# Kernel optimization log

Hardware: AMD Instinct MI355X
Metric: run time of the kernel (lower is better)

Reference implementation:

```python
import jax, jax.numpy as jnp
import numpy as np
from jax import lax

HIDDEN = 256
HORIZON = 168  # 7 * 24


def _cell(x, h, c, Wih, Whh, bih, bhh):
    # PyTorch LSTM cell: gate order i, f, g, o
    gates = x @ Wih.T + bih + h @ Whh.T + bhh  # [B, 4*HIDDEN]
    i, f, g, o = jnp.split(gates, 4, axis=-1)
    c = jax.nn.sigmoid(f) * c + jax.nn.sigmoid(i) * jnp.tanh(g)
    h = jax.nn.sigmoid(o) * jnp.tanh(c)
    return h, c


def setup_inputs() -> dict:
    key = jax.random.key(0)
    ks = jax.random.split(key, 20)
    B, T, H = 1024, 336, HIDDEN
    s = 0.05

    def p(k, shape):
        return jax.random.normal(k, shape, dtype=jnp.float32) * s

    inp = {"x": jax.random.normal(ks[0], (B, T), dtype=jnp.float32)}
    # encoder layer 0 (input_size=1), layer 1 (input=HIDDEN)
    inp["enc_Wih0"] = p(ks[1], (4 * H, 1)); inp["enc_Whh0"] = p(ks[2], (4 * H, H))
    inp["enc_bih0"] = p(ks[3], (4 * H,)); inp["enc_bhh0"] = p(ks[4], (4 * H,))
    inp["enc_Wih1"] = p(ks[5], (4 * H, H)); inp["enc_Whh1"] = p(ks[6], (4 * H, H))
    inp["enc_bih1"] = p(ks[7], (4 * H,)); inp["enc_bhh1"] = p(ks[8], (4 * H,))
    # decoder layers
    inp["dec_Wih0"] = p(ks[9], (4 * H, 1)); inp["dec_Whh0"] = p(ks[10], (4 * H, H))
    inp["dec_bih0"] = p(ks[11], (4 * H,)); inp["dec_bhh0"] = p(ks[12], (4 * H,))
    inp["dec_Wih1"] = p(ks[13], (4 * H, H)); inp["dec_Whh1"] = p(ks[14], (4 * H, H))
    inp["dec_bih1"] = p(ks[15], (4 * H,)); inp["dec_bhh1"] = p(ks[16], (4 * H,))
    # final projection hidden -> 1
    inp["fc_W"] = p(ks[17], (1, H)); inp["fc_b"] = p(ks[18], (1,))
    return inp


def reference(x, enc_Wih0, enc_Whh0, enc_bih0, enc_bhh0,
              enc_Wih1, enc_Whh1, enc_bih1, enc_bhh1,
              dec_Wih0, dec_Whh0, dec_bih0, dec_bhh0,
              dec_Wih1, dec_Whh1, dec_bih1, dec_bhh1,
              fc_W, fc_b):
    B = x.shape[0]
    xs = x[:, :, None].transpose(1, 0, 2)  # [T, B, 1]
    z = jnp.zeros((B, HIDDEN), dtype=x.dtype)

    def enc_step(carry, xt):
        h0, c0, h1, c1 = carry
        h0, c0 = _cell(xt, h0, c0, enc_Wih0, enc_Whh0, enc_bih0, enc_bhh0)
        h1, c1 = _cell(h0, h1, c1, enc_Wih1, enc_Whh1, enc_bih1, enc_bhh1)
        return (h0, c0, h1, c1), None

    (h0, c0, h1, c1), _ = lax.scan(enc_step, (z, z, z, z), xs)

    dec_inp = x[:, -1:]  # [B, 1] last observed value

    def dec_step(carry, _):
        h0, c0, h1, c1, inp = carry
        h0, c0 = _cell(inp, h0, c0, dec_Wih0, dec_Whh0, dec_bih0, dec_bhh0)
        h1, c1 = _cell(h0, h1, c1, dec_Wih1, dec_Whh1, dec_bih1, dec_bhh1)
        pred = h1 @ fc_W.T + fc_b  # [B, 1]
        return (h0, c0, h1, c1, pred), pred

    _, preds = lax.scan(dec_step, (h0, c0, h1, c1, dec_inp), None, length=HORIZON)
    return preds[:, :, 0].T  # [B, HORIZON]
```

## Files before the change

kernel.cpp:

```cpp
#include <hip/hip_runtime.h>

#define HIDDEN 256
#define TENC 336
#define HORIZ 168
#define BSZ 1024
#define BH (BSZ*HIDDEN)

typedef _Float16 f16;
typedef f16 f16x8 __attribute__((ext_vector_type(8)));
typedef float f32x4 __attribute__((ext_vector_type(4)));
typedef unsigned int u32;
typedef unsigned long long u64;

#define H0_OFF 0
#define H1_OFF (2*BH*2)
#define PP_OFF (H1_OFF + 2*BH*2)
#define CNT_OFF (PP_OFF + BSZ*16*4)
#define WS_TOTAL (CNT_OFF + 16*128)

#define LDS_A0 0
#define LDS_A1 32768
#define LDS_X0 65536
#define XSTRIDE 18
#define LDS_X1 (LDS_X0 + 256*XSTRIDE*4)
#define LDS_SM (LDS_X1 + 256*XSTRIDE*4)
#define LDS_TOTAL (LDS_SM + 1024)

__device__ __forceinline__ float sigm(float x){ return 1.0f/(1.0f+__expf(-x)); }
__device__ __forceinline__ float tanh_f(float x){ return 2.0f/(1.0f+__expf(-2.0f*x)) - 1.0f; }

__device__ __forceinline__ u64 ald64(const void* p){
  return __hip_atomic_load((const u64*)p, __ATOMIC_RELAXED, __HIP_MEMORY_SCOPE_AGENT);
}
__device__ __forceinline__ u32 ald32(const u32* p){
  return __hip_atomic_load(p, __ATOMIC_RELAXED, __HIP_MEMORY_SCOPE_AGENT);
}
__device__ __forceinline__ void ast32(u32* p, u32 v){
  __hip_atomic_store(p, v, __ATOMIC_RELAXED, __HIP_MEMORY_SCOPE_AGENT);
}

__device__ __forceinline__ f16x8 loadWfrag(const float* W, int grow, int k){
  const float* p = W + grow*HIDDEN + k;
  float4 lo = *(const float4*)p;
  float4 hi = *(const float4*)(p+4);
  f16x8 r;
  r[0]=(f16)lo.x; r[1]=(f16)lo.y; r[2]=(f16)lo.z; r[3]=(f16)lo.w;
  r[4]=(f16)hi.x; r[5]=(f16)hi.y; r[6]=(f16)hi.z; r[7]=(f16)hi.w;
  return r;
}

__device__ __forceinline__ const f16* slot_src(const f16* base, int g, int s){
  int l = s & 63, f = s >> 6;
  int kt = f >> 2, mt = f & 3;
  int row = g*64 + mt*16 + (l&15);
  int k = kt*32 + 8*(l>>4);
  return base + row*HIDDEN + k;
}

__device__ __forceinline__ void stage_tile(char* dst, const f16* src_base, int g, int tid){
  u64 v[8];
  #pragma unroll
  for (int i=0;i<4;++i){
    const f16* src = slot_src(src_base, g, tid + 512*i);
    v[2*i]   = ald64(src);
    v[2*i+1] = ald64(src+4);
  }
  #pragma unroll
  for (int i=0;i<4;++i){
    int s = tid + 512*i;
    *(u64*)(dst + s*16)     = v[2*i];
    *(u64*)(dst + s*16 + 8) = v[2*i+1];
  }
}

__device__ __forceinline__ void stage2(char* dA, const f16* sA, char* dB, const f16* sB,
                                       int g, int tid){
  u64 va[8], vb[8];
  #pragma unroll
  for (int i=0;i<4;++i){
    const f16* src = slot_src(sA, g, tid + 512*i);
    va[2*i]   = ald64(src);
    va[2*i+1] = ald64(src+4);
  }
  #pragma unroll
  for (int i=0;i<4;++i){
    const f16* src = slot_src(sB, g, tid + 512*i);
    vb[2*i]   = ald64(src);
    vb[2*i+1] = ald64(src+4);
  }
  #pragma unroll
  for (int i=0;i<4;++i){
    int s = tid + 512*i;
    *(u64*)(dA + s*16)     = va[2*i];
    *(u64*)(dA + s*16 + 8) = va[2*i+1];
    *(u64*)(dB + s*16)     = vb[2*i];
    *(u64*)(dB + s*16 + 8) = vb[2*i+1];
  }
}

__device__ __forceinline__ void cellpair(const float* X, const float* bs, const float* wih, float xr,
                                         int crow, int dp, float& ca, float& cb, float& hA, float& hB){
  float iA = X[(0*64+crow)*XSTRIDE+dp  ] + bs[dp]      + xr*wih[dp];
  float iB = X[(0*64+crow)*XSTRIDE+dp+1] + bs[dp+1]    + xr*wih[dp+1];
  float fA = X[(1*64+crow)*XSTRIDE+dp  ] + bs[16+dp]   + xr*wih[16+dp];
  float fB = X[(1*64+crow)*XSTRIDE+dp+1] + bs[16+dp+1] + xr*wih[16+dp+1];
  float gA = X[(2*64+crow)*XSTRIDE+dp  ] + bs[32+dp]   + xr*wih[32+dp];
  float gB = X[(2*64+crow)*XSTRIDE+dp+1] + bs[32+dp+1] + xr*wih[32+dp+1];
  float oA = X[(3*64+crow)*XSTRIDE+dp  ] + bs[48+dp]   + xr*wih[48+dp];
  float oB = X[(3*64+crow)*XSTRIDE+dp+1] + bs[48+dp+1] + xr*wih[48+dp+1];
  ca = sigm(fA)*ca + sigm(iA)*tanh_f(gA);
  cb = sigm(fB)*cb + sigm(iB)*tanh_f(gB);
  hA = sigm(oA)*tanh_f(ca);
  hB = sigm(oB)*tanh_f(cb);
}

__device__ __forceinline__ void storeh(f16* base, int rowg, int col, float hA, float hB){
  u32 pk = (u32)__builtin_bit_cast(unsigned short, (f16)hA)
         | ((u32)__builtin_bit_cast(unsigned short, (f16)hB) << 16);
  ast32((u32*)(base + rowg*HIDDEN + col), pk);
}

__device__ __forceinline__ void gbar(u32* cnt, int tid, u32 target){
  __syncthreads();
  if (tid == 0)
    (void)__hip_atomic_fetch_add(cnt, 1u, __ATOMIC_RELAXED, __HIP_MEMORY_SCOPE_AGENT);
  if (tid < 64){
    for (int it = 0; it < (1<<17); ++it){
      if (ald32(cnt) >= target) break;
    }
  }
  __syncthreads();
}

struct P {
  const float *x;
  const float *eWih0,*eWhh0,*eBih0,*eBhh0,*eWih1,*eWhh1,*eBih1,*eBhh1;
  const float *dWih0,*dWhh0,*dBih0,*dBhh0,*dWih1,*dWhh1,*dBih1,*dBhh1;
  const float *fcW,*fcB;
  float* out;
  char* ws;
};

__global__ void initk(char* ws){
  u32* p = (u32*)ws;
  size_t total = (size_t)WS_TOTAL / 4;
  for (size_t k = (size_t)blockIdx.x*blockDim.x + threadIdx.x; k < total;
       k += (size_t)gridDim.x*blockDim.x) p[k] = 0u;
}

__global__ __launch_bounds__(512, 2) void lstm_main(P p){
  const int tid  = threadIdx.x;
  const int lane = tid & 63;
  const int w    = tid >> 6;
  const int n    = w & 3;
  const int mh   = w >> 2;
  const int blk  = blockIdx.x;
  const int g    = blk & 15;
  const int j    = blk >> 4;

  extern __shared__ __align__(16) char smem[];
  char*  A0 = smem + LDS_A0;
  char*  A1 = smem + LDS_A1;
  float* X0 = (float*)(smem + LDS_X0);
  float* X1 = (float*)(smem + LDS_X1);
  float* wih0s = (float*)(smem + LDS_SM);
  float* b0s   = wih0s + 64;
  float* b1s   = wih0s + 128;
  float* fcWs  = wih0s + 192;
  float* fcbs  = wih0s + 208;

  f16*   h0buf = (f16*)(p.ws + H0_OFF);
  f16*   h1buf = (f16*)(p.ws + H1_OFF);
  float* ppart = (float*)(p.ws + PP_OFF);
  u32*   cnt   = (u32*)(p.ws + CNT_OFF) + g*32;

  const int crow = tid >> 3;
  const int dp   = (tid & 7) * 2;
  const int rowg = g*64 + crow;
  const int cold = j*16 + dp;

  float c0a=0.f, c0b=0.f, c1a=0.f, c1b=0.f;

  if (tid < 64){
    int gt = tid >> 4, d = tid & 15;
    int grow = gt*256 + j*16 + d;
    wih0s[tid] = p.eWih0[grow];
    b0s[tid] = p.eBih0[grow] + p.eBhh0[grow];
    b1s[tid] = p.eBih1[grow] + p.eBhh1[grow];
  }
  if (tid < 16) fcWs[tid] = p.fcW[j*16 + tid];
  if (tid == 0) fcbs[0] = p.fcB[0];

  f16x8 B0[8], B1i[8], B1h[8];
  {
    int grow = n*256 + j*16 + (lane & 15);
    int kb = 8*(lane>>4);
    #pragma unroll
    for (int kt=0; kt<8; ++kt){
      B0[kt]  = loadWfrag(p.eWhh0, grow, kt*32 + kb);
      B1i[kt] = loadWfrag(p.eWih1, grow, kt*32 + kb);
      B1h[kt] = loadWfrag(p.eWhh1, grow, kt*32 + kb);
    }
  }
  __syncthreads();

  u32 ev = 0;

  for (int r = 0; r <= TENC; ++r){
    float xr = (r < TENC) ? p.x[rowg*TENC + r] : 0.f;
    stage2(A0, h0buf + ((r+1)&1)*BH, A1, h1buf + (r&1)*BH, g, tid);
    __syncthreads();

    f32x4 acc0[2] = {{0.f,0.f,0.f,0.f},{0.f,0.f,0.f,0.f}};
    f32x4 acc1[2] = {{0.f,0.f,0.f,0.f},{0.f,0.f,0.f,0.f}};
    #pragma unroll
    for (int kt=0; kt<8; ++kt){
      #pragma unroll
      for (int m=0; m<2; ++m){
        f16x8 a = *(const f16x8*)(A0 + ((kt*4 + (mh*2+m))*64 + lane)*16);
        acc0[m] = __builtin_amdgcn_mfma_f32_16x16x32_f16(a, B0[kt],  acc0[m], 0,0,0);
        acc1[m] = __builtin_amdgcn_mfma_f32_16x16x32_f16(a, B1i[kt], acc1[m], 0,0,0);
      }
    }
    #pragma unroll
    for (int kt=0; kt<8; ++kt){
      #pragma unroll
      for (int m=0; m<2; ++m){
        f16x8 a = *(const f16x8*)(A1 + ((kt*4 + (mh*2+m))*64 + lane)*16);
        acc1[m] = __builtin_amdgcn_mfma_f32_16x16x32_f16(a, B1h[kt], acc1[m], 0,0,0);
      }
    }

    #pragma unroll
    for (int m=0; m<2; ++m){
      int rb = mh*32 + m*16 + 4*(lane>>4);
      #pragma unroll
      for (int q=0; q<4; ++q){
        X0[(n*64 + rb + q)*XSTRIDE + (lane&15)] = acc0[m][q];
        X1[(n*64 + rb + q)*XSTRIDE + (lane&15)] = acc1[m][q];
      }
    }
    __syncthreads();

    if (r < TENC){
      float hA, hB;
      cellpair(X0, b0s, wih0s, xr, crow, dp, c0a, c0b, hA, hB);
      storeh(h0buf + (r&1)*BH, rowg, cold, hA, hB);
    }
    if (r >= 1){
      float hA, hB;
      cellpair(X1, b1s, wih0s, 0.f, crow, dp, c1a, c1b, hA, hB);
      storeh(h1buf + ((r-1)&1)*BH, rowg, cold, hA, hB);
    }
    ++ev;
    gbar(cnt, tid, 16u*ev);
  }

  __syncthreads();
  if (tid < 64){
    int gt = tid >> 4, d = tid & 15;
    int grow = gt*256 + j*16 + d;
    wih0s[tid] = p.dWih0[grow];
    b0s[tid] = p.dBih0[grow] + p.dBhh0[grow];
    b1s[tid] = p.dBih1[grow] + p.dBhh1[grow];
  }
  {
    int grow = n*256 + j*16 + (lane & 15);
    int kb = 8*(lane>>4);
    #pragma unroll
    for (int kt=0; kt<8; ++kt){
      B0[kt]  = loadWfrag(p.dWhh0, grow, kt*32 + kb);
      B1i[kt] = loadWfrag(p.dWih1, grow, kt*32 + kb);
      B1h[kt] = loadWfrag(p.dWhh1, grow, kt*32 + kb);
    }
  }
  __syncthreads();

  for (int t = 0; t < HORIZ; ++t){
    u64 ppv = 0;
    float xlast = 0.f;
    if (t == 0) xlast = p.x[rowg*TENC + (TENC-1)];
    else        ppv   = ald64(ppart + rowg*16 + (tid&7)*2);

    stage2(A0, h0buf + ((t+1)&1)*BH, A1, h1buf + ((t+1)&1)*BH, g, tid);
    __syncthreads();

    f32x4 acc0[2] = {{0.f,0.f,0.f,0.f},{0.f,0.f,0.f,0.f}};
    f32x4 acc1[2] = {{0.f,0.f,0.f,0.f},{0.f,0.f,0.f,0.f}};
    #pragma unroll
    for (int kt=0; kt<8; ++kt){
      #pragma unroll
      for (int m=0; m<2; ++m){
        f16x8 a0 = *(const f16x8*)(A0 + ((kt*4 + (mh*2+m))*64 + lane)*16);
        acc0[m] = __builtin_amdgcn_mfma_f32_16x16x32_f16(a0, B0[kt],  acc0[m], 0,0,0);
        f16x8 a1 = *(const f16x8*)(A1 + ((kt*4 + (mh*2+m))*64 + lane)*16);
        acc1[m] = __builtin_amdgcn_mfma_f32_16x16x32_f16(a1, B1h[kt], acc1[m], 0,0,0);
      }
    }
    #pragma unroll
    for (int m=0; m<2; ++m){
      int rb = mh*32 + m*16 + 4*(lane>>4);
      #pragma unroll
      for (int q=0; q<4; ++q) X0[(n*64 + rb + q)*XSTRIDE + (lane&15)] = acc0[m][q];
    }
    __syncthreads();

    float inp;
    if (t == 0){
      inp = xlast;
    } else {
      float a = __builtin_bit_cast(float, (u32)(ppv & 0xffffffffull));
      float b = __builtin_bit_cast(float, (u32)(ppv >> 32));
      float s = a + b;
      s += __shfl_xor(s, 1);
      s += __shfl_xor(s, 2);
      s += __shfl_xor(s, 4);
      inp = s + fcbs[0];
    }
    {
      float hA, hB;
      cellpair(X0, b0s, wih0s, inp, crow, dp, c0a, c0b, hA, hB);
      storeh(h0buf + (t&1)*BH, rowg, cold, hA, hB);
    }
    if (t > 0 && j == 0 && (tid & 7) == 0) p.out[rowg*HORIZ + (t-1)] = inp;
    ++ev;
    gbar(cnt, tid, 16u*ev);

    stage_tile(A0, h0buf + (t&1)*BH, g, tid);
    __syncthreads();

    #pragma unroll
    for (int kt=0; kt<8; ++kt){
      #pragma unroll
      for (int m=0; m<2; ++m){
        f16x8 a0 = *(const f16x8*)(A0 + ((kt*4 + (mh*2+m))*64 + lane)*16);
        acc1[m] = __builtin_amdgcn_mfma_f32_16x16x32_f16(a0, B1i[kt], acc1[m], 0,0,0);
      }
    }
    #pragma unroll
    for (int m=0; m<2; ++m){
      int rb = mh*32 + m*16 + 4*(lane>>4);
      #pragma unroll
      for (int q=0; q<4; ++q) X1[(n*64 + rb + q)*XSTRIDE + (lane&15)] = acc1[m][q];
    }
    __syncthreads();

    {
      float hA, hB;
      cellpair(X1, b1s, wih0s, 0.f, crow, dp, c1a, c1b, hA, hB);
      storeh(h1buf + (t&1)*BH, rowg, cold, hA, hB);
      float pp = fcWs[dp]*hA + fcWs[dp+1]*hB;
      pp += __shfl_xor(pp, 1);
      pp += __shfl_xor(pp, 2);
      pp += __shfl_xor(pp, 4);
      if ((tid & 7) == 0)
        ast32((u32*)(ppart + rowg*16 + j), __builtin_bit_cast(u32, pp));
    }
    ++ev;
    gbar(cnt, tid, 16u*ev);
  }

  if (j == 0){
    u64 ppv = ald64(ppart + rowg*16 + (tid&7)*2);
    float a = __builtin_bit_cast(float, (u32)(ppv & 0xffffffffull));
    float b = __builtin_bit_cast(float, (u32)(ppv >> 32));
    float s = a + b;
    s += __shfl_xor(s, 1);
    s += __shfl_xor(s, 2);
    s += __shfl_xor(s, 4);
    if ((tid & 7) == 0) p.out[rowg*HORIZ + (HORIZ-1)] = s + fcbs[0];
  }
}

extern "C" void kernel_launch(void* const* d_in, const int* in_sizes, int n_in,
                              void* d_out, int out_size, void* d_ws, size_t ws_size,
                              hipStream_t stream) {
  (void)in_sizes; (void)n_in; (void)out_size;
  if (ws_size < (size_t)WS_TOTAL) return;

  P prm;
  prm.x     = (const float*)d_in[0];
  prm.eWih0 = (const float*)d_in[1];  prm.eWhh0 = (const float*)d_in[2];
  prm.eBih0 = (const float*)d_in[3];  prm.eBhh0 = (const float*)d_in[4];
  prm.eWih1 = (const float*)d_in[5];  prm.eWhh1 = (const float*)d_in[6];
  prm.eBih1 = (const float*)d_in[7];  prm.eBhh1 = (const float*)d_in[8];
  prm.dWih0 = (const float*)d_in[9];  prm.dWhh0 = (const float*)d_in[10];
  prm.dBih0 = (const float*)d_in[11]; prm.dBhh0 = (const float*)d_in[12];
  prm.dWih1 = (const float*)d_in[13]; prm.dWhh1 = (const float*)d_in[14];
  prm.dBih1 = (const float*)d_in[15]; prm.dBhh1 = (const float*)d_in[16];
  prm.fcW   = (const float*)d_in[17]; prm.fcB   = (const float*)d_in[18];
  prm.out   = (float*)d_out;
  prm.ws    = (char*)d_ws;

  hipLaunchKernelGGL(initk, dim3(512), dim3(256), 0, stream, (char*)d_ws);

  hipFuncSetAttribute((const void*)lstm_main,
                      hipFuncAttributeMaxDynamicSharedMemorySize, LDS_TOTAL);
  void* args[] = { &prm };
  hipLaunchCooperativeKernel((const void*)lstm_main, dim3(256), dim3(512),
                             args, LDS_TOTAL, stream);
}
```

Baseline: 4.034 ms.

## Replace atomic-counter barrier with per-block flags and pre-convert weights to fp16

```diff
diff --git a/kernel.cpp b/kernel.cpp
--- a/kernel.cpp
+++ b/kernel.cpp
@@ -5,6 +5,7 @@
 #define HORIZ 168
 #define BSZ 1024
 #define BH (BSZ*HIDDEN)
+#define WMAT (1024*256)
 
 typedef _Float16 f16;
 typedef f16 f16x8 __attribute__((ext_vector_type(8)));
@@ -15,13 +16,15 @@
 #define H0_OFF 0
 #define H1_OFF (2*BH*2)
 #define PP_OFF (H1_OFF + 2*BH*2)
-#define CNT_OFF (PP_OFF + BSZ*16*4)
-#define WS_TOTAL (CNT_OFF + 16*128)
+#define FLAG_OFF (PP_OFF + BSZ*16*4)
+#define WS_BASE (FLAG_OFF + 16*16*64)
+#define WF16_OFF WS_BASE
+#define WS_FULL (WF16_OFF + 6*WMAT*2)
 
 #define LDS_A0 0
 #define LDS_A1 32768
 #define LDS_X0 65536
-#define XSTRIDE 18
+#define XSTRIDE 16
 #define LDS_X1 (LDS_X0 + 256*XSTRIDE*4)
 #define LDS_SM (LDS_X1 + 256*XSTRIDE*4)
 #define LDS_TOTAL (LDS_SM + 1024)
@@ -120,13 +123,13 @@
   ast32((u32*)(base + rowg*HIDDEN + col), pk);
 }
 
-__device__ __forceinline__ void gbar(u32* cnt, int tid, u32 target){
+__device__ __forceinline__ void gbar(u32* gf, int j, int lane, int tid, u32 ev){
   __syncthreads();
-  if (tid == 0)
-    (void)__hip_atomic_fetch_add(cnt, 1u, __ATOMIC_RELAXED, __HIP_MEMORY_SCOPE_AGENT);
-  if (tid < 64){
+  if (tid == 0) ast32(gf + j*16, ev);
+  if (tid < 64 && lane < 16){
+    const u32* sp = gf + lane*16;
     for (int it = 0; it < (1<<17); ++it){
-      if (ald32(cnt) >= target) break;
+      if (__all((int)(ald32(sp) >= ev))) break;
     }
   }
   __syncthreads();
@@ -139,16 +142,32 @@
   const float *fcW,*fcB;
   float* out;
   char* ws;
+  int usef16;
+};
+
+struct WC {
+  const float* src0; const float* src1; const float* src2;
+  const float* src3; const float* src4; const float* src5;
+  f16* dst;
 };
 
 __global__ void initk(char* ws){
   u32* p = (u32*)ws;
-  size_t total = (size_t)WS_TOTAL / 4;
+  size_t total = (size_t)WS_BASE / 4;
   for (size_t k = (size_t)blockIdx.x*blockDim.x + threadIdx.x; k < total;
        k += (size_t)gridDim.x*blockDim.x) p[k] = 0u;
 }
 
-__global__ __launch_bounds__(512, 2) void lstm_main(P p){
+__global__ void wconv(WC wc){
+  int m = blockIdx.y;
+  const float* s = (m==0)?wc.src0:(m==1)?wc.src1:(m==2)?wc.src2:
+                   (m==3)?wc.src3:(m==4)?wc.src4:wc.src5;
+  f16* d = wc.dst + (size_t)m*WMAT;
+  for (int i = blockIdx.x*blockDim.x + threadIdx.x; i < WMAT;
+       i += gridDim.x*blockDim.x) d[i] = (f16)s[i];
+}
+
+__global__ __launch_bounds__(512) void lstm_main(P p){
   const int tid  = threadIdx.x;
   const int lane = tid & 63;
   const int w    = tid >> 6;
@@ -172,7 +191,8 @@
   f16*   h0buf = (f16*)(p.ws + H0_OFF);
   f16*   h1buf = (f16*)(p.ws + H1_OFF);
   float* ppart = (float*)(p.ws + PP_OFF);
-  u32*   cnt   = (u32*)(p.ws + CNT_OFF) + g*32;
+  u32*   gf    = (u32*)(p.ws + FLAG_OFF) + g*256;
+  const f16* wf = (const f16*)(p.ws + WF16_OFF);
 
   const int crow = tid >> 3;
   const int dp   = (tid & 7) * 2;
@@ -191,10 +211,18 @@
   if (tid < 16) fcWs[tid] = p.fcW[j*16 + tid];
   if (tid == 0) fcbs[0] = p.fcB[0];
 
+  const int grow = n*256 + j*16 + (lane & 15);
+  const int kb = 8*(lane>>4);
   f16x8 B0[8], B1i[8], B1h[8];
-  {
-    int grow = n*256 + j*16 + (lane & 15);
-    int kb = 8*(lane>>4);
+  if (p.usef16){
+    #pragma unroll
+    for (int kt=0; kt<8; ++kt){
+      int ko = kt*32 + kb;
+      B0[kt]  = *(const f16x8*)(wf + 0*WMAT + grow*HIDDEN + ko);
+      B1i[kt] = *(const f16x8*)(wf + 1*WMAT + grow*HIDDEN + ko);
+      B1h[kt] = *(const f16x8*)(wf + 2*WMAT + grow*HIDDEN + ko);
+    }
+  } else {
     #pragma unroll
     for (int kt=0; kt<8; ++kt){
       B0[kt]  = loadWfrag(p.eWhh0, grow, kt*32 + kb);
@@ -253,20 +281,26 @@
       storeh(h1buf + ((r-1)&1)*BH, rowg, cold, hA, hB);
     }
     ++ev;
-    gbar(cnt, tid, 16u*ev);
+    gbar(gf, j, lane, tid, ev);
   }
 
   __syncthreads();
   if (tid < 64){
     int gt = tid >> 4, d = tid & 15;
-    int grow = gt*256 + j*16 + d;
-    wih0s[tid] = p.dWih0[grow];
-    b0s[tid] = p.dBih0[grow] + p.dBhh0[grow];
-    b1s[tid] = p.dBih1[grow] + p.dBhh1[grow];
-  }
-  {
-    int grow = n*256 + j*16 + (lane & 15);
-    int kb = 8*(lane>>4);
+    int grw = gt*256 + j*16 + d;
+    wih0s[tid] = p.dWih0[grw];
+    b0s[tid] = p.dBih0[grw] + p.dBhh0[grw];
+    b1s[tid] = p.dBih1[grw] + p.dBhh1[grw];
+  }
+  if (p.usef16){
+    #pragma unroll
+    for (int kt=0; kt<8; ++kt){
+      int ko = kt*32 + kb;
+      B0[kt]  = *(const f16x8*)(wf + 3*WMAT + grow*HIDDEN + ko);
+      B1i[kt] = *(const f16x8*)(wf + 4*WMAT + grow*HIDDEN + ko);
+      B1h[kt] = *(const f16x8*)(wf + 5*WMAT + grow*HIDDEN + ko);
+    }
+  } else {
     #pragma unroll
     for (int kt=0; kt<8; ++kt){
       B0[kt]  = loadWfrag(p.dWhh0, grow, kt*32 + kb);
@@ -324,7 +358,7 @@
     }
     if (t > 0 && j == 0 && (tid & 7) == 0) p.out[rowg*HORIZ + (t-1)] = inp;
     ++ev;
-    gbar(cnt, tid, 16u*ev);
+    gbar(gf, j, lane, tid, ev);
 
     stage_tile(A0, h0buf + (t&1)*BH, g, tid);
     __syncthreads();
@@ -357,7 +391,7 @@
         ast32((u32*)(ppart + rowg*16 + j), __builtin_bit_cast(u32, pp));
     }
     ++ev;
-    gbar(cnt, tid, 16u*ev);
+    gbar(gf, j, lane, tid, ev);
   }
 
   if (j == 0){
@@ -376,7 +410,8 @@
                               void* d_out, int out_size, void* d_ws, size_t ws_size,
                               hipStream_t stream) {
   (void)in_sizes; (void)n_in; (void)out_size;
-  if (ws_size < (size_t)WS_TOTAL) return;
+  if (ws_size < (size_t)WS_BASE) return;
+  const int usef16 = (ws_size >= (size_t)WS_FULL) ? 1 : 0;
 
   P prm;
   prm.x     = (const float*)d_in[0];
@@ -391,8 +426,17 @@
   prm.fcW   = (const float*)d_in[17]; prm.fcB   = (const float*)d_in[18];
   prm.out   = (float*)d_out;
   prm.ws    = (char*)d_ws;
-
-  hipLaunchKernelGGL(initk, dim3(512), dim3(256), 0, stream, (char*)d_ws);
+  prm.usef16 = usef16;
+
+  hipLaunchKernelGGL(initk, dim3(256), dim3(256), 0, stream, (char*)d_ws);
+
+  if (usef16){
+    WC wc;
+    wc.src0 = prm.eWhh0; wc.src1 = prm.eWih1; wc.src2 = prm.eWhh1;
+    wc.src3 = prm.dWhh0; wc.src4 = prm.dWih1; wc.src5 = prm.dWhh1;
+    wc.dst  = (f16*)((char*)d_ws + WF16_OFF);
+    hipLaunchKernelGGL(wconv, dim3(128, 6), dim3(256), 0, stream, wc);
+  }
 
   hipFuncSetAttribute((const void*)lstm_main,
                       hipFuncAttributeMaxDynamicSharedMemorySize, LDS_TOTAL);
```

New measurement: 4.385 ms. 1.09x slower.
